# Kernel optimization log

Hardware: AMD Instinct MI355X
Metric: run time of the kernel (lower is better)

The kernel has to match this reference:

```python
import jax, jax.numpy as jnp
import numpy as np
import math

EMB = 768
B, S = 8, 2048

def setup_inputs() -> dict:
    key = jax.random.key(0)
    ks = jax.random.split(key, 6)
    q = jax.random.normal(ks[0], (B, S, EMB), dtype=jnp.float32)
    k = jax.random.normal(ks[1], (B, S, EMB), dtype=jnp.float32)
    v = jax.random.normal(ks[2], (B, S, EMB), dtype=jnp.float32)
    mask = jax.random.randint(ks[3], (B, S, S), 0, 2, dtype=jnp.int32)
    # nn.Linear(emb, emb): weight [out, in], bias [out]
    bound = 1.0 / math.sqrt(EMB)
    W = jax.random.uniform(ks[4], (EMB, EMB), minval=-bound, maxval=bound, dtype=jnp.float32)
    b = jax.random.uniform(ks[5], (EMB,), minval=-bound, maxval=bound, dtype=jnp.float32)
    return {"q": q, "k": k, "v": v, "mask": mask, "W": W, "b": b}

def reference(q, k, v, mask, W, b):
    # shared linear projection (torch Linear: x @ W^T + b)
    qp = jnp.einsum('bse,oe->bso', q, W) + b
    kp = jnp.einsum('bse,oe->bso', k, W) + b
    vp = jnp.einsum('bse,oe->bso', v, W) + b
    scores = jnp.einsum('bqe,bke->bqk', qp, kp) / math.sqrt(EMB)  # [B,S,S]
    scores = jnp.where(mask == 1, -jnp.inf, scores)
    attn = jax.nn.softmax(scores, axis=-1)
    return jnp.einsum('bqk,bke->bqe', attn, vp)
```

## Files before the change

### kernel.cpp

```cpp
#include <hip/hip_runtime.h>
#include <hip/hip_bf16.h>
#include <stdint.h>

#define B_ 8
#define S_ 2048
#define E_ 768

typedef __attribute__((ext_vector_type(4))) float f32x4;
typedef __attribute__((ext_vector_type(8))) short bf16x8;


__device__ __forceinline__ unsigned pk2bf(float x, float y) {
  unsigned r;
  asm("v_cvt_pk_bf16_f32 %0, %1, %2" : "=v"(r) : "v"(x), "v"(y));
  return r;
}

__device__ __forceinline__ void gll16(const void* g, void* l) {
  __builtin_amdgcn_global_load_lds((const __attribute__((address_space(1))) void*)g,
                                   (__attribute__((address_space(3))) void*)l, 16, 0, 0);
}

__device__ __forceinline__ void gemm128(const char* __restrict__ Ab,
                                        const char* __restrict__ Bb,
                                        int ldA, int ldB, int NT,
                                        unsigned short* As, unsigned short* Bs,
                                        int tid, int wm, int wn, int lane,
                                        f32x4 (&acc)[4][4]) {
  unsigned sA[2], sB[2], lin2[2];
#pragma unroll
  for (int i = 0; i < 2; ++i) {
    const unsigned lin = (unsigned)i * 4096u + (unsigned)tid * 16u;
    const unsigned row = lin >> 6, ch = (lin >> 4) & 3u;
    const unsigned sw = (ch ^ ((row >> 1) & 3u)) << 4;
    sA[i] = row * (unsigned)ldA + sw;
    sB[i] = row * (unsigned)ldB + sw;
    lin2[i] = lin;
  }
  unsigned aoff[4], boff[4];
#pragma unroll
  for (int m = 0; m < 4; ++m) {
    unsigned row = (unsigned)(wm * 64 + m * 16 + (lane & 15));
    aoff[m] = row * 64 + ((((unsigned)lane >> 4) ^ ((row >> 1) & 3u)) << 4);
    row = (unsigned)(wn * 64 + m * 16 + (lane & 15));
    boff[m] = row * 64 + ((((unsigned)lane >> 4) ^ ((row >> 1) & 3u)) << 4);
  }
#pragma unroll
  for (int i = 0; i < 2; ++i) {
    gll16(Ab + sA[i], (char*)As + lin2[i]);
    gll16(Bb + sB[i], (char*)Bs + lin2[i]);
  }
  asm volatile("s_waitcnt vmcnt(0)" ::: "memory");
  __builtin_amdgcn_s_barrier();
  __builtin_amdgcn_sched_barrier(0);
  for (int kt = 0; kt < NT; ++kt) {
    const char* Ac = (const char*)As + (kt & 1) * 8192;
    const char* Bc = (const char*)Bs + (kt & 1) * 8192;
    char* An = (char*)As + ((kt + 1) & 1) * 8192;
    char* Bn = (char*)Bs + ((kt + 1) & 1) * 8192;
    if (kt + 1 < NT) {
      const size_t ko = (size_t)(kt + 1) * 64;
#pragma unroll
      for (int i = 0; i < 2; ++i) {
        gll16(Ab + sA[i] + ko, An + lin2[i]);
        gll16(Bb + sB[i] + ko, Bn + lin2[i]);
      }
    }
    bf16x8 af[4], bf[4];
#pragma unroll
    for (int m = 0; m < 4; ++m) af[m] = *reinterpret_cast<const bf16x8*>(Ac + aoff[m]);
#pragma unroll
    for (int n = 0; n < 4; ++n) bf[n] = *reinterpret_cast<const bf16x8*>(Bc + boff[n]);
    asm volatile("s_waitcnt lgkmcnt(0)" ::: "memory");
    __builtin_amdgcn_sched_barrier(0);
    __builtin_amdgcn_s_setprio(1);
#pragma unroll
    for (int m = 0; m < 4; ++m)
#pragma unroll
      for (int n = 0; n < 4; ++n)
        acc[m][n] = __builtin_amdgcn_mfma_f32_16x16x32_bf16(af[m], bf[n], acc[m][n], 0, 0, 0);
    __builtin_amdgcn_s_setprio(0);
    if (kt + 1 < NT) {
      asm volatile("s_waitcnt vmcnt(0)" ::: "memory");
      __builtin_amdgcn_s_barrier();
      __builtin_amdgcn_sched_barrier(0);
    }
  }
}

__global__ __launch_bounds__(256) void k_cvt(const float* __restrict__ q,
                                             const float* __restrict__ k,
                                             const float* __restrict__ v,
                                             const float* __restrict__ W,
                                             const int* __restrict__ mask,
                                             unsigned short* __restrict__ qb,
                                             unsigned short* __restrict__ kb,
                                             unsigned short* __restrict__ vb,
                                             unsigned short* __restrict__ Wb,
                                             unsigned long long* __restrict__ mwords) {
  const int y = blockIdx.y;
  if (y == 4) {
    const int nchunks = B_ * S_ * (S_ / 256);
    const int lane = threadIdx.x & 63;
    const int wave = (blockIdx.x * 256 + threadIdx.x) >> 6;
    const int nw = gridDim.x * 4;
    int c = wave;
    for (; c + 3 * nw < nchunks; c += 4 * nw) {
      int4 v0 = *reinterpret_cast<const int4*>(&mask[(size_t)c * 256 + lane * 4]);
      int4 v1 = *reinterpret_cast<const int4*>(&mask[(size_t)(c + nw) * 256 + lane * 4]);
      int4 v2 = *reinterpret_cast<const int4*>(&mask[(size_t)(c + 2 * nw) * 256 + lane * 4]);
      int4 v3 = *reinterpret_cast<const int4*>(&mask[(size_t)(c + 3 * nw) * 256 + lane * 4]);
      unsigned long long a0 = __ballot(v0.x == 1), a1 = __ballot(v0.y == 1);
      unsigned long long a2 = __ballot(v0.z == 1), a3 = __ballot(v0.w == 1);
      unsigned long long b0 = __ballot(v1.x == 1), b1 = __ballot(v1.y == 1);
      unsigned long long b2 = __ballot(v1.z == 1), b3 = __ballot(v1.w == 1);
      unsigned long long c0 = __ballot(v2.x == 1), c1 = __ballot(v2.y == 1);
      unsigned long long c2 = __ballot(v2.z == 1), c3 = __ballot(v2.w == 1);
      unsigned long long d0 = __ballot(v3.x == 1), d1 = __ballot(v3.y == 1);
      unsigned long long d2 = __ballot(v3.z == 1), d3 = __ballot(v3.w == 1);
      if (lane == 0) {
        *reinterpret_cast<ulonglong2*>(&mwords[(size_t)c * 4]) = make_ulonglong2(a0, a1);
        *reinterpret_cast<ulonglong2*>(&mwords[(size_t)c * 4 + 2]) = make_ulonglong2(a2, a3);
        *reinterpret_cast<ulonglong2*>(&mwords[(size_t)(c + nw) * 4]) = make_ulonglong2(b0, b1);
        *reinterpret_cast<ulonglong2*>(&mwords[(size_t)(c + nw) * 4 + 2]) = make_ulonglong2(b2, b3);
        *reinterpret_cast<ulonglong2*>(&mwords[(size_t)(c + 2 * nw) * 4]) = make_ulonglong2(c0, c1);
        *reinterpret_cast<ulonglong2*>(&mwords[(size_t)(c + 2 * nw) * 4 + 2]) = make_ulonglong2(c2, c3);
        *reinterpret_cast<ulonglong2*>(&mwords[(size_t)(c + 3 * nw) * 4]) = make_ulonglong2(d0, d1);
        *reinterpret_cast<ulonglong2*>(&mwords[(size_t)(c + 3 * nw) * 4 + 2]) = make_ulonglong2(d2, d3);
      }
    }
    for (; c < nchunks; c += nw) {
      int4 v0 = *reinterpret_cast<const int4*>(&mask[(size_t)c * 256 + lane * 4]);
      unsigned long long a0 = __ballot(v0.x == 1), a1 = __ballot(v0.y == 1);
      unsigned long long a2 = __ballot(v0.z == 1), a3 = __ballot(v0.w == 1);
      if (lane == 0) {
        *reinterpret_cast<ulonglong2*>(&mwords[(size_t)c * 4]) = make_ulonglong2(a0, a1);
        *reinterpret_cast<ulonglong2*>(&mwords[(size_t)c * 4 + 2]) = make_ulonglong2(a2, a3);
      }
    }
    return;
  }
  const float* src = (y == 0) ? q : (y == 1) ? k : (y == 2) ? v : W;
  unsigned short* dst = (y == 0) ? qb : (y == 1) ? kb : (y == 2) ? vb : Wb;
  const int n4 = (y < 3) ? (B_ * S_ * E_ / 4) : (E_ * E_ / 4);
  const int stride = gridDim.x * 256;
  const float4* s4 = reinterpret_cast<const float4*>(src);
  uint2* d2 = reinterpret_cast<uint2*>(dst);
  int i = blockIdx.x * 256 + threadIdx.x;
  for (; i + 3 * stride < n4; i += 4 * stride) {
    float4 f0 = s4[i];
    float4 f1 = s4[i + stride];
    float4 f2 = s4[i + 2 * stride];
    float4 f3 = s4[i + 3 * stride];
    d2[i]              = make_uint2(pk2bf(f0.x, f0.y), pk2bf(f0.z, f0.w));
    d2[i + stride]     = make_uint2(pk2bf(f1.x, f1.y), pk2bf(f1.z, f1.w));
    d2[i + 2 * stride] = make_uint2(pk2bf(f2.x, f2.y), pk2bf(f2.z, f2.w));
    d2[i + 3 * stride] = make_uint2(pk2bf(f3.x, f3.y), pk2bf(f3.z, f3.w));
  }
  for (; i < n4; i += stride) {
    float4 f0 = s4[i];
    d2[i] = make_uint2(pk2bf(f0.x, f0.y), pk2bf(f0.z, f0.w));
  }
}

__global__ __launch_bounds__(256, 3) void k_projb(const unsigned short* __restrict__ Xb,
                                                  const unsigned short* __restrict__ Wb,
                                                  const float* __restrict__ bias,
                                                  unsigned short* __restrict__ qp,
                                                  unsigned short* __restrict__ kp,
                                                  unsigned short* __restrict__ vp) {
  __shared__ __attribute__((aligned(16))) unsigned short As[2 * 4096];
  __shared__ __attribute__((aligned(16))) unsigned short Bs[2 * 4096];
  const int tid = threadIdx.x, lane = tid & 63, wid = tid >> 6;
  const int wm = wid >> 1, wn = wid & 1;
  const int c0 = blockIdx.x * 128, r0 = blockIdx.y * 128, z = blockIdx.z;
  const unsigned short* X = Xb + (size_t)z * (B_ * S_ * E_);
  unsigned short* O = (z == 0) ? qp : ((z == 1) ? kp : vp);

  f32x4 acc[4][4] = {};
  gemm128((const char*)(X + (size_t)r0 * E_), (const char*)(Wb + (size_t)c0 * E_),
          E_ * 2, E_ * 2, E_ / 32, As, Bs, tid, wm, wn, lane, acc);

  float bcol[4];
#pragma unroll
  for (int n = 0; n < 4; ++n) bcol[n] = bias[c0 + wn * 64 + n * 16 + (lane & 15)];
#pragma unroll
  for (int m = 0; m < 4; ++m)
#pragma unroll
    for (int r = 0; r < 4; ++r) {
      const int row = r0 + wm * 64 + m * 16 + (lane >> 4) * 4 + r;
#pragma unroll
      for (int n = 0; n < 4; ++n) {
        const int col = c0 + wn * 64 + n * 16 + (lane & 15);
        O[(size_t)row * E_ + col] = (unsigned short)pk2bf(acc[m][n][r] + bcol[n], 0.f);
      }
    }
}

__global__ __launch_bounds__(256) void k_vtrans(const unsigned short* __restrict__ vp,
                                                unsigned short* __restrict__ vpT) {
  __shared__ __attribute__((aligned(16))) unsigned short t[64][72];
  const int tid = threadIdx.x;
  const int st = blockIdx.x;
  const int ot = blockIdx.y;
  const int b = blockIdx.z;
#pragma unroll
  for (int i = 0; i < 2; ++i) {
    int f = i * 256 + tid;
    int s = f >> 3, c8 = f & 7;
    uint4 vv = *reinterpret_cast<const uint4*>(
        &vp[((size_t)b * S_ + st * 64 + s) * E_ + ot * 64 + c8 * 8]);
    *reinterpret_cast<uint4*>(&t[s][c8 * 8]) = vv;
  }
  __syncthreads();
  const int o = tid >> 2;
  const int sb = (tid & 3) * 16;
  unsigned p[8];
#pragma unroll
  for (int j = 0; j < 8; ++j)
    p[j] = (unsigned)t[sb + 2 * j][o] | ((unsigned)t[sb + 2 * j + 1][o] << 16);
  uint4 w0 = make_uint4(p[0], p[1], p[2], p[3]);
  uint4 w1 = make_uint4(p[4], p[5], p[6], p[7]);
  size_t ob = ((size_t)b * E_ + ot * 64 + o) * S_ + st * 64 + sb;
  *reinterpret_cast<uint4*>(&vpT[ob]) = w0;
  *reinterpret_cast<uint4*>(&vpT[ob + 8]) = w1;
}

__global__ __launch_bounds__(256, 3) void k_scores(const unsigned short* __restrict__ qp,
                                                   const unsigned short* __restrict__ kp,
                                                   const unsigned long long* __restrict__ mwords,
                                                   unsigned short* __restrict__ P,
                                                   float* __restrict__ rowsum) {
  __shared__ __attribute__((aligned(16))) unsigned short As[2 * 4096];
  __shared__ __attribute__((aligned(16))) unsigned short Bs[2 * 4096];
  __shared__ float rlds[128][2];
  const int tid = threadIdx.x, lane = tid & 63, wid = tid >> 6;
  const int wm = wid >> 1, wn = wid & 1;
  const int yt = blockIdx.x, qt = blockIdx.y, b = blockIdx.z;
  f32x4 acc[4][4] = {};
  gemm128((const char*)(qp + ((size_t)b * S_ + qt * 128) * E_),
          (const char*)(kp + ((size_t)b * S_ + yt * 128) * E_),
          E_ * 2, E_ * 2, E_ / 32, As, Bs, tid, wm, wn, lane, acc);

  const float SC = (float)(1.4426950408889634 / 27.712812921102035);
#pragma unroll
  for (int m = 0; m < 4; ++m)
#pragma unroll
    for (int r = 0; r < 4; ++r) {
      const int rloc = wm * 64 + m * 16 + (lane >> 4) * 4 + r;
      const int grow = qt * 128 + rloc;
      const size_t rowoff = ((size_t)b * S_ + grow) * S_;
      const unsigned long long mw =
          mwords[(((size_t)b * S_ + grow) * 8 + (yt >> 1)) * 4 + (lane & 3)];
      const int shb = (yt & 1) * 32 + wn * 16 + ((lane & 15) >> 2);
      const int cbase = yt * 128 + wn * 64 + (lane & 15);
      float radd = 0.f;
#pragma unroll
      for (int n = 0; n < 4; ++n) {
        float pv = ((mw >> (shb + n * 4)) & 1ull)
                       ? 0.f
                       : __builtin_amdgcn_exp2f(acc[m][n][r] * SC);
        radd += pv;
        P[rowoff + cbase + n * 16] = (unsigned short)pk2bf(pv, 0.f);
      }
      float vsum = radd;
      vsum += __shfl_xor(vsum, 1);
      vsum += __shfl_xor(vsum, 2);
      vsum += __shfl_xor(vsum, 4);
      vsum += __shfl_xor(vsum, 8);
      if ((lane & 15) == 0) rlds[rloc][wn] = vsum;
    }
  __syncthreads();
  if (tid < 128) {
    rowsum[(size_t)yt * (B_ * S_) + (size_t)b * S_ + qt * 128 + tid] =
        rlds[tid][0] + rlds[tid][1];
  }
}

__global__ __launch_bounds__(256) void k_invrs(const float* __restrict__ rowsum,
                                               float* __restrict__ inv_rs) {
  int i = blockIdx.x * 256 + threadIdx.x;
  float t = 0.f;
#pragma unroll
  for (int g = 0; g < 16; ++g) t += rowsum[(size_t)g * (B_ * S_) + i];
  inv_rs[i] = 1.0f / t;
}

__global__ __launch_bounds__(256, 3) void k_pv(const unsigned short* __restrict__ P,
                                               const unsigned short* __restrict__ vpT,
                                               const float* __restrict__ inv_rs,
                                               float* __restrict__ out) {
  __shared__ __attribute__((aligned(16))) unsigned short As[2 * 4096];
  __shared__ __attribute__((aligned(16))) unsigned short Bs[2 * 4096];
  const int tid = threadIdx.x, lane = tid & 63, wid = tid >> 6;
  const int wm = wid >> 1, wn = wid & 1;
  const int et = blockIdx.x, mt = blockIdx.y, b = blockIdx.z;
  f32x4 acc[4][4] = {};
  gemm128((const char*)(P + ((size_t)b * S_ + mt * 128) * S_),
          (const char*)(vpT + ((size_t)b * E_ + et * 128) * S_),
          S_ * 2, S_ * 2, S_ / 32, As, Bs, tid, wm, wn, lane, acc);

#pragma unroll
  for (int m = 0; m < 4; ++m)
#pragma unroll
    for (int r = 0; r < 4; ++r) {
      const int grow = mt * 128 + wm * 64 + m * 16 + (lane >> 4) * 4 + r;
      const float inv = inv_rs[b * S_ + grow];
#pragma unroll
      for (int n = 0; n < 4; ++n) {
        const int col = et * 128 + wn * 64 + n * 16 + (lane & 15);
        out[((size_t)b * S_ + grow) * E_ + col] = acc[m][n][r] * inv;
      }
    }
}

extern "C" void kernel_launch(void* const* d_in, const int* in_sizes, int n_in,
                              void* d_out, int out_size, void* d_ws, size_t ws_size,
                              hipStream_t stream) {
  const float* q = (const float*)d_in[0];
  const float* k = (const float*)d_in[1];
  const float* v = (const float*)d_in[2];
  const int* mask = (const int*)d_in[3];
  const float* W = (const float*)d_in[4];
  const float* bias = (const float*)d_in[5];
  float* out = (float*)d_out;
  char* ws = (char*)d_ws;

  unsigned short* qb = (unsigned short*)(ws + 0);
  unsigned short* kb = (unsigned short*)(ws + 25165824);
  unsigned short* vb = (unsigned short*)(ws + 50331648);
  unsigned short* Wb = (unsigned short*)(ws + 75497472);
  unsigned short* qp = (unsigned short*)(ws + 76677120);
  unsigned short* kp = (unsigned short*)(ws + 101842944);
  unsigned short* vpT = (unsigned short*)(ws + 127008768);
  unsigned short* P = (unsigned short*)(ws + 0);
  float* rowsum = (float*)(ws + 75497472);
  float* inv_rs = (float*)(ws + 76546048);
  unsigned short* vp_tmp = (unsigned short*)d_out;
  unsigned long long* mwords =
      (unsigned long long*)((char*)d_out + 25165824);
  (void)in_sizes; (void)n_in; (void)out_size; (void)ws_size;

  dim3 blk(256, 1, 1);
  k_cvt<<<dim3(512, 5, 1), blk, 0, stream>>>(q, k, v, W, mask, qb, kb, vb, Wb, mwords);
  k_projb<<<dim3(6, 128, 3), blk, 0, stream>>>(qb, Wb, bias, qp, kp, vp_tmp);
  k_vtrans<<<dim3(32, 12, 8), blk, 0, stream>>>(vp_tmp, vpT);
  k_scores<<<dim3(16, 16, 8), blk, 0, stream>>>(qp, kp, mwords, P, rowsum);
  k_invrs<<<dim3(64, 1, 1), blk, 0, stream>>>(rowsum, inv_rs);
  k_pv<<<dim3(6, 16, 8), blk, 0, stream>>>(P, vpT, inv_rs, out);
}
```

Measured before the change: 351.9 us.

## Split conversion kernel and add XCD-aware block swizzle to GEMM kernels

The combined fp32-to-bf16 and mask-packing kernel is split into three kernels: one grid-sized q/k/v converter with no loop, one W converter, and one mask packer with more blocks. The projection, scores and PV GEMM kernels now launch 1D grids and remap block ids so that consecutive ids, which are spread round-robin across the 8 XCDs, map to contiguous tiles on each XCD. This is meant to improve L2 reuse of shared operand rows per XCD. It adds extra kernel launches and loses the overlap of mask packing with conversion inside one launch.

```diff
diff --git a/kernel.cpp b/kernel.cpp
--- a/kernel.cpp
+++ b/kernel.cpp
@@ -88,78 +88,74 @@
   }
 }
 
-__global__ __launch_bounds__(256) void k_cvt(const float* __restrict__ q,
-                                             const float* __restrict__ k,
-                                             const float* __restrict__ v,
-                                             const float* __restrict__ W,
-                                             const int* __restrict__ mask,
-                                             unsigned short* __restrict__ qb,
-                                             unsigned short* __restrict__ kb,
-                                             unsigned short* __restrict__ vb,
-                                             unsigned short* __restrict__ Wb,
-                                             unsigned long long* __restrict__ mwords) {
-  const int y = blockIdx.y;
-  if (y == 4) {
-    const int nchunks = B_ * S_ * (S_ / 256);
-    const int lane = threadIdx.x & 63;
-    const int wave = (blockIdx.x * 256 + threadIdx.x) >> 6;
-    const int nw = gridDim.x * 4;
-    int c = wave;
-    for (; c + 3 * nw < nchunks; c += 4 * nw) {
-      int4 v0 = *reinterpret_cast<const int4*>(&mask[(size_t)c * 256 + lane * 4]);
-      int4 v1 = *reinterpret_cast<const int4*>(&mask[(size_t)(c + nw) * 256 + lane * 4]);
-      int4 v2 = *reinterpret_cast<const int4*>(&mask[(size_t)(c + 2 * nw) * 256 + lane * 4]);
-      int4 v3 = *reinterpret_cast<const int4*>(&mask[(size_t)(c + 3 * nw) * 256 + lane * 4]);
-      unsigned long long a0 = __ballot(v0.x == 1), a1 = __ballot(v0.y == 1);
-      unsigned long long a2 = __ballot(v0.z == 1), a3 = __ballot(v0.w == 1);
-      unsigned long long b0 = __ballot(v1.x == 1), b1 = __ballot(v1.y == 1);
-      unsigned long long b2 = __ballot(v1.z == 1), b3 = __ballot(v1.w == 1);
-      unsigned long long c0 = __ballot(v2.x == 1), c1 = __ballot(v2.y == 1);
-      unsigned long long c2 = __ballot(v2.z == 1), c3 = __ballot(v2.w == 1);
-      unsigned long long d0 = __ballot(v3.x == 1), d1 = __ballot(v3.y == 1);
-      unsigned long long d2 = __ballot(v3.z == 1), d3 = __ballot(v3.w == 1);
-      if (lane == 0) {
-        *reinterpret_cast<ulonglong2*>(&mwords[(size_t)c * 4]) = make_ulonglong2(a0, a1);
-        *reinterpret_cast<ulonglong2*>(&mwords[(size_t)c * 4 + 2]) = make_ulonglong2(a2, a3);
-        *reinterpret_cast<ulonglong2*>(&mwords[(size_t)(c + nw) * 4]) = make_ulonglong2(b0, b1);
-        *reinterpret_cast<ulonglong2*>(&mwords[(size_t)(c + nw) * 4 + 2]) = make_ulonglong2(b2, b3);
-        *reinterpret_cast<ulonglong2*>(&mwords[(size_t)(c + 2 * nw) * 4]) = make_ulonglong2(c0, c1);
-        *reinterpret_cast<ulonglong2*>(&mwords[(size_t)(c + 2 * nw) * 4 + 2]) = make_ulonglong2(c2, c3);
-        *reinterpret_cast<ulonglong2*>(&mwords[(size_t)(c + 3 * nw) * 4]) = make_ulonglong2(d0, d1);
-        *reinterpret_cast<ulonglong2*>(&mwords[(size_t)(c + 3 * nw) * 4 + 2]) = make_ulonglong2(d2, d3);
-      }
-    }
-    for (; c < nchunks; c += nw) {
-      int4 v0 = *reinterpret_cast<const int4*>(&mask[(size_t)c * 256 + lane * 4]);
-      unsigned long long a0 = __ballot(v0.x == 1), a1 = __ballot(v0.y == 1);
-      unsigned long long a2 = __ballot(v0.z == 1), a3 = __ballot(v0.w == 1);
-      if (lane == 0) {
-        *reinterpret_cast<ulonglong2*>(&mwords[(size_t)c * 4]) = make_ulonglong2(a0, a1);
-        *reinterpret_cast<ulonglong2*>(&mwords[(size_t)c * 4 + 2]) = make_ulonglong2(a2, a3);
-      }
-    }
-    return;
-  }
-  const float* src = (y == 0) ? q : (y == 1) ? k : (y == 2) ? v : W;
-  unsigned short* dst = (y == 0) ? qb : (y == 1) ? kb : (y == 2) ? vb : Wb;
-  const int n4 = (y < 3) ? (B_ * S_ * E_ / 4) : (E_ * E_ / 4);
-  const int stride = gridDim.x * 256;
+__global__ __launch_bounds__(256) void k_cvt3(const float* __restrict__ q,
+                                              const float* __restrict__ k,
+                                              const float* __restrict__ v,
+                                              unsigned short* __restrict__ qb,
+                                              unsigned short* __restrict__ kb,
+                                              unsigned short* __restrict__ vb) {
+  const int z = blockIdx.y;
+  const float* src = (z == 0) ? q : (z == 1) ? k : v;
+  unsigned short* dst = (z == 0) ? qb : (z == 1) ? kb : vb;
+  const int i0 = blockIdx.x * 512 + threadIdx.x;
   const float4* s4 = reinterpret_cast<const float4*>(src);
   uint2* d2 = reinterpret_cast<uint2*>(dst);
-  int i = blockIdx.x * 256 + threadIdx.x;
-  for (; i + 3 * stride < n4; i += 4 * stride) {
-    float4 f0 = s4[i];
-    float4 f1 = s4[i + stride];
-    float4 f2 = s4[i + 2 * stride];
-    float4 f3 = s4[i + 3 * stride];
-    d2[i]              = make_uint2(pk2bf(f0.x, f0.y), pk2bf(f0.z, f0.w));
-    d2[i + stride]     = make_uint2(pk2bf(f1.x, f1.y), pk2bf(f1.z, f1.w));
-    d2[i + 2 * stride] = make_uint2(pk2bf(f2.x, f2.y), pk2bf(f2.z, f2.w));
-    d2[i + 3 * stride] = make_uint2(pk2bf(f3.x, f3.y), pk2bf(f3.z, f3.w));
-  }
-  for (; i < n4; i += stride) {
-    float4 f0 = s4[i];
-    d2[i] = make_uint2(pk2bf(f0.x, f0.y), pk2bf(f0.z, f0.w));
+  float4 f0 = s4[i0];
+  float4 f1 = s4[i0 + 256];
+  d2[i0]       = make_uint2(pk2bf(f0.x, f0.y), pk2bf(f0.z, f0.w));
+  d2[i0 + 256] = make_uint2(pk2bf(f1.x, f1.y), pk2bf(f1.z, f1.w));
+}
+
+__global__ __launch_bounds__(256) void k_cvtW(const float* __restrict__ W,
+                                              unsigned short* __restrict__ Wb) {
+  const int i0 = blockIdx.x * 512 + threadIdx.x;
+  const float4* s4 = reinterpret_cast<const float4*>(W);
+  uint2* d2 = reinterpret_cast<uint2*>(Wb);
+  float4 f0 = s4[i0];
+  float4 f1 = s4[i0 + 256];
+  d2[i0]       = make_uint2(pk2bf(f0.x, f0.y), pk2bf(f0.z, f0.w));
+  d2[i0 + 256] = make_uint2(pk2bf(f1.x, f1.y), pk2bf(f1.z, f1.w));
+}
+
+__global__ __launch_bounds__(256) void k_pack(const int* __restrict__ mask,
+                                              unsigned long long* __restrict__ mwords) {
+  const int nchunks = B_ * S_ * (S_ / 256);
+  const int lane = threadIdx.x & 63;
+  const int wave = (blockIdx.x * 256 + threadIdx.x) >> 6;
+  const int nw = gridDim.x * 4;
+  int c = wave;
+  for (; c + 3 * nw < nchunks; c += 4 * nw) {
+    int4 v0 = *reinterpret_cast<const int4*>(&mask[(size_t)c * 256 + lane * 4]);
+    int4 v1 = *reinterpret_cast<const int4*>(&mask[(size_t)(c + nw) * 256 + lane * 4]);
+    int4 v2 = *reinterpret_cast<const int4*>(&mask[(size_t)(c + 2 * nw) * 256 + lane * 4]);
+    int4 v3 = *reinterpret_cast<const int4*>(&mask[(size_t)(c + 3 * nw) * 256 + lane * 4]);
+    unsigned long long a0 = __ballot(v0.x == 1), a1 = __ballot(v0.y == 1);
+    unsigned long long a2 = __ballot(v0.z == 1), a3 = __ballot(v0.w == 1);
+    unsigned long long b0 = __ballot(v1.x == 1), b1 = __ballot(v1.y == 1);
+    unsigned long long b2 = __ballot(v1.z == 1), b3 = __ballot(v1.w == 1);
+    unsigned long long c0 = __ballot(v2.x == 1), c1 = __ballot(v2.y == 1);
+    unsigned long long c2 = __ballot(v2.z == 1), c3 = __ballot(v2.w == 1);
+    unsigned long long d0 = __ballot(v3.x == 1), d1 = __ballot(v3.y == 1);
+    unsigned long long d2 = __ballot(v3.z == 1), d3 = __ballot(v3.w == 1);
+    if (lane == 0) {
+      *reinterpret_cast<ulonglong2*>(&mwords[(size_t)c * 4]) = make_ulonglong2(a0, a1);
+      *reinterpret_cast<ulonglong2*>(&mwords[(size_t)c * 4 + 2]) = make_ulonglong2(a2, a3);
+      *reinterpret_cast<ulonglong2*>(&mwords[(size_t)(c + nw) * 4]) = make_ulonglong2(b0, b1);
+      *reinterpret_cast<ulonglong2*>(&mwords[(size_t)(c + nw) * 4 + 2]) = make_ulonglong2(b2, b3);
+      *reinterpret_cast<ulonglong2*>(&mwords[(size_t)(c + 2 * nw) * 4]) = make_ulonglong2(c0, c1);
+      *reinterpret_cast<ulonglong2*>(&mwords[(size_t)(c + 2 * nw) * 4 + 2]) = make_ulonglong2(c2, c3);
+      *reinterpret_cast<ulonglong2*>(&mwords[(size_t)(c + 3 * nw) * 4]) = make_ulonglong2(d0, d1);
+      *reinterpret_cast<ulonglong2*>(&mwords[(size_t)(c + 3 * nw) * 4 + 2]) = make_ulonglong2(d2, d3);
+    }
+  }
+  for (; c < nchunks; c += nw) {
+    int4 v0 = *reinterpret_cast<const int4*>(&mask[(size_t)c * 256 + lane * 4]);
+    unsigned long long a0 = __ballot(v0.x == 1), a1 = __ballot(v0.y == 1);
+    unsigned long long a2 = __ballot(v0.z == 1), a3 = __ballot(v0.w == 1);
+    if (lane == 0) {
+      *reinterpret_cast<ulonglong2*>(&mwords[(size_t)c * 4]) = make_ulonglong2(a0, a1);
+      *reinterpret_cast<ulonglong2*>(&mwords[(size_t)c * 4 + 2]) = make_ulonglong2(a2, a3);
+    }
   }
 }
 
@@ -173,7 +169,11 @@
   __shared__ __attribute__((aligned(16))) unsigned short Bs[2 * 4096];
   const int tid = threadIdx.x, lane = tid & 63, wid = tid >> 6;
   const int wm = wid >> 1, wn = wid & 1;
-  const int c0 = blockIdx.x * 128, r0 = blockIdx.y * 128, z = blockIdx.z;
+  const int id = blockIdx.x;
+  const int swz = (id & 7) * 288 + (id >> 3);
+  const int z = swz / 768;
+  const int rem = swz - z * 768;
+  const int r0 = (rem / 6) * 128, c0 = (rem % 6) * 128;
   const unsigned short* X = Xb + (size_t)z * (B_ * S_ * E_);
   unsigned short* O = (z == 0) ? qp : ((z == 1) ? kp : vp);
 
@@ -236,7 +236,10 @@
   __shared__ float rlds[128][2];
   const int tid = threadIdx.x, lane = tid & 63, wid = tid >> 6;
   const int wm = wid >> 1, wn = wid & 1;
-  const int yt = blockIdx.x, qt = blockIdx.y, b = blockIdx.z;
+  const int id = blockIdx.x;
+  const int swz = (id & 7) * 256 + (id >> 3);
+  const int b = swz >> 8;
+  const int qt = (swz >> 4) & 15, yt = swz & 15;
   f32x4 acc[4][4] = {};
   gemm128((const char*)(qp + ((size_t)b * S_ + qt * 128) * E_),
           (const char*)(kp + ((size_t)b * S_ + yt * 128) * E_),
@@ -294,7 +297,11 @@
   __shared__ __attribute__((aligned(16))) unsigned short Bs[2 * 4096];
   const int tid = threadIdx.x, lane = tid & 63, wid = tid >> 6;
   const int wm = wid >> 1, wn = wid & 1;
-  const int et = blockIdx.x, mt = blockIdx.y, b = blockIdx.z;
+  const int id = blockIdx.x;
+  const int swz = (id & 7) * 96 + (id >> 3);
+  const int b = swz / 96;
+  const int rem = swz - b * 96;
+  const int mt = rem / 6, et = rem % 6;
   f32x4 acc[4][4] = {};
   gemm128((const char*)(P + ((size_t)b * S_ + mt * 128) * S_),
           (const char*)(vpT + ((size_t)b * E_ + et * 128) * S_),
@@ -342,10 +349,12 @@
   (void)in_sizes; (void)n_in; (void)out_size; (void)ws_size;
 
   dim3 blk(256, 1, 1);
-  k_cvt<<<dim3(512, 5, 1), blk, 0, stream>>>(q, k, v, W, mask, qb, kb, vb, Wb, mwords);
-  k_projb<<<dim3(6, 128, 3), blk, 0, stream>>>(qb, Wb, bias, qp, kp, vp_tmp);
+  k_cvt3<<<dim3(6144, 3, 1), blk, 0, stream>>>(q, k, v, qb, kb, vb);
+  k_cvtW<<<dim3(288, 1, 1), blk, 0, stream>>>(W, Wb);
+  k_pack<<<dim3(2048, 1, 1), blk, 0, stream>>>(mask, mwords);
+  k_projb<<<dim3(2304, 1, 1), blk, 0, stream>>>(qb, Wb, bias, qp, kp, vp_tmp);
   k_vtrans<<<dim3(32, 12, 8), blk, 0, stream>>>(vp_tmp, vpT);
-  k_scores<<<dim3(16, 16, 8), blk, 0, stream>>>(qp, kp, mwords, P, rowsum);
+  k_scores<<<dim3(2048, 1, 1), blk, 0, stream>>>(qp, kp, mwords, P, rowsum);
   k_invrs<<<dim3(64, 1, 1), blk, 0, stream>>>(rowsum, inv_rs);
-  k_pv<<<dim3(6, 16, 8), blk, 0, stream>>>(P, vpT, inv_rs, out);
-}
+  k_pv<<<dim3(768, 1, 1), blk, 0, stream>>>(P, vpT, inv_rs, out);
+}
```

New measurement: 309.3 us. 12.1% less time.
